# Kernel optimization log

Measured on AMD Instinct MI355X. Metric: run time of the kernel, lower is better.

Reference implementation:

```python
import jax, jax.numpy as jnp
import numpy as np

B, N, C = 2, 2048, 1024
H = 16
D = C // H  # head_dim = 64
SCALE = D ** -0.5


def setup_inputs() -> dict:
    key = jax.random.key(0)
    ks = jax.random.split(key, 9)
    s = C ** -0.5  # ~ torch Linear default init scale
    return {
        "x": jax.random.normal(ks[0], (B, N, C), dtype=jnp.float32),
        "Wq": jax.random.uniform(ks[1], (C, C), jnp.float32, -s, s),
        "bq": jax.random.uniform(ks[2], (C,), jnp.float32, -s, s),
        "Wk": jax.random.uniform(ks[3], (C, C), jnp.float32, -s, s),
        "bk": jax.random.uniform(ks[4], (C,), jnp.float32, -s, s),
        "Wv": jax.random.uniform(ks[5], (C, C), jnp.float32, -s, s),
        "bv": jax.random.uniform(ks[6], (C,), jnp.float32, -s, s),
        "Wo": jax.random.uniform(ks[7], (C, C), jnp.float32, -s, s),
        "bo": jax.random.uniform(ks[8], (C,), jnp.float32, -s, s),
    }


def reference(x, Wq, bq, Wk, bk, Wv, bv, Wo, bo):
    # Projections: [B,N,C] -> [B,H,N,D]
    def split_heads(t):
        return t.reshape(B, N, H, D).transpose(0, 2, 1, 3)

    q = split_heads(x @ Wq.T + bq)
    k = split_heads(x @ Wk.T + bk)
    v = split_heads(x @ Wv.T + bv)

    scores = jnp.einsum("bhnd,bhmd->bhnm", q, k) * SCALE  # [B,H,N,N]
    attn = jax.nn.softmax(scores, axis=-1)
    out = jnp.einsum("bhnm,bhmd->bhnd", attn, v)  # [B,H,N,D]
    out = out.transpose(0, 2, 1, 3).reshape(B, N, C)
    return out @ Wo.T + bo
```

## Files before the change

### kernel.cpp

```cpp
#include <hip/hip_runtime.h>
#include <stdint.h>


typedef _Float16 h8 __attribute__((ext_vector_type(8)));
typedef _Float16 h4 __attribute__((ext_vector_type(4)));
typedef float f4 __attribute__((ext_vector_type(4)));
typedef float f16f __attribute__((ext_vector_type(16)));
typedef uint32_t u32;
typedef u32 u32x4 __attribute__((ext_vector_type(4)));

#define AS1(p) ((const __attribute__((address_space(1))) void*)(p))
#define AS3(p) ((__attribute__((address_space(3))) void*)(p))

template <int ITERS>
__device__ __forceinline__ void stage128B(const _Float16* g, int ldk, _Float16* s, int tid) {
#pragma unroll
  for (int j = 0; j < ITERS; ++j) {
    int off = j * 4096 + tid * 16;
    int row = off >> 7;
    int ch = (off >> 4) & 7;
    int gch = ch ^ (row & 7);
    __builtin_amdgcn_global_load_lds(AS1(g + row * ldk + gch * 8), AS3(s + (off >> 1)), 16, 0, 0);
  }
}

__device__ __forceinline__ void stage_v(const _Float16* g, _Float16* s, int tid) {
#pragma unroll
  for (int j = 0; j < 2; ++j) {
    int off = j * 4096 + tid * 16;
    int row = off >> 7;
    int ch = (off >> 4) & 7;
    int gch = ch ^ (row & 7);
    __builtin_amdgcn_global_load_lds(AS1(g + row * 2048 + gch * 8), AS3(s + (off >> 1)), 16, 0, 0);
  }
}
__device__ __forceinline__ void stage_k(const _Float16* g, _Float16* s, int tid) {
#pragma unroll
  for (int j = 0; j < 2; ++j) {
    int off = j * 4096 + tid * 16;
    int row = off >> 7;
    int ch = (off >> 4) & 7;
    int gch = ch ^ ((row & 3) | ((row >> 1) & 4));
    __builtin_amdgcn_global_load_lds(AS1(g + row * 64 + gch * 8), AS3(s + (off >> 1)), 16, 0, 0);
  }
}

__device__ __forceinline__ h8 frag64(const _Float16* s, int row, int g) {
  return *(const h8*)(s + row * 64 + ((g ^ (row & 7)) << 3));
}

__global__ void cvt_all(const float* __restrict__ x, const float* __restrict__ Wq,
                        const float* __restrict__ Wk, const float* __restrict__ Wv,
                        const float* __restrict__ Wo, _Float16* __restrict__ xh,
                        _Float16* __restrict__ q, _Float16* __restrict__ k,
                        _Float16* __restrict__ v, _Float16* __restrict__ o) {
  int blk = blockIdx.x;
  const float* src; _Float16* dst; int off;
  if (blk < 4096)      { src = x;  dst = xh; off = blk; }
  else if (blk < 5120) { src = Wq; dst = q;  off = blk - 4096; }
  else if (blk < 6144) { src = Wk; dst = k;  off = blk - 5120; }
  else if (blk < 7168) { src = Wv; dst = v;  off = blk - 6144; }
  else                 { src = Wo; dst = o;  off = blk - 7168; }
  int i = off * 1024 + threadIdx.x * 4;
  f4 vv = *(const f4*)(src + i);
  h4 ov;
  ov[0] = (_Float16)vv[0]; ov[1] = (_Float16)vv[1]; ov[2] = (_Float16)vv[2]; ov[3] = (_Float16)vv[3];
  *(h4*)(dst + i) = ov;
}

__global__ __launch_bounds__(256, 3) void gemm_qkv(
    const _Float16* __restrict__ X,
    const _Float16* __restrict__ W0, const _Float16* __restrict__ W1, const _Float16* __restrict__ W2,
    const float* __restrict__ b0, const float* __restrict__ b1, const float* __restrict__ b2,
    _Float16* __restrict__ O0, _Float16* __restrict__ O1, _Float16* __restrict__ O2) {
  __shared__ _Float16 As[128 * 64];
  __shared__ _Float16 Bs[128 * 64];
  int z = blockIdx.z;
  const _Float16* W = (z == 0) ? W0 : (z == 1) ? W1 : W2;
  const float* bias = (z == 0) ? b0 : (z == 1) ? b1 : b2;

  int tid = threadIdx.x;
  int lane = tid & 63, wave = tid >> 6;
  int quad = lane >> 4, l15 = lane & 15;
  int wm = (wave >> 1) << 6, wn = (wave & 1) << 6;
  int m0 = blockIdx.y << 7, n0 = blockIdx.x << 7;

  f4 acc[4][4] = {};
  for (int k0 = 0; k0 < 1024; k0 += 64) {
    stage128B<4>(X + m0 * 1024 + k0, 1024, As, tid);
    stage128B<4>(W + n0 * 1024 + k0, 1024, Bs, tid);
    __syncthreads();
#pragma unroll
    for (int ks = 0; ks < 2; ++ks) {
      h8 af[4], bf[4];
#pragma unroll
      for (int i = 0; i < 4; ++i) af[i] = frag64(As, wm + i * 16 + l15, ks * 4 + quad);
#pragma unroll
      for (int i = 0; i < 4; ++i) bf[i] = frag64(Bs, wn + i * 16 + l15, ks * 4 + quad);
#pragma unroll
      for (int mi = 0; mi < 4; ++mi)
#pragma unroll
        for (int ni = 0; ni < 4; ++ni)
          acc[mi][ni] = __builtin_amdgcn_mfma_f32_16x16x32_f16(af[mi], bf[ni], acc[mi][ni], 0, 0, 0);
    }
    __syncthreads();
  }

  if (z == 2) {
#pragma unroll
    for (int mi = 0; mi < 4; ++mi) {
#pragma unroll
      for (int ni = 0; ni < 4; ++ni) {
        int o = n0 + wn + ni * 16 + l15;
        float bv = bias[o];
        int h = o >> 6, dd = o & 63;
        int m = m0 + wm + mi * 16 + quad * 4;
        int b = m >> 11, n = m & 2047;
        h4 v;
#pragma unroll
        for (int r = 0; r < 4; ++r) v[r] = (_Float16)(acc[mi][ni][r] + bv);
        *(h4*)(O2 + (((b * 16 + h) * 64 + dd) * 2048 + n)) = v;
      }
    }
  } else {
    float scale = (z == 0) ? 0.125f * 1.44269504089f : 1.0f;
    _Float16* Out = (z == 0) ? O0 : O1;
#pragma unroll
    for (int mi = 0; mi < 4; ++mi) {
#pragma unroll
      for (int ni = 0; ni < 4; ++ni) {
        int o = n0 + wn + ni * 16 + l15;
        float bv = bias[o];
        int h = o >> 6, d = o & 63;
#pragma unroll
        for (int r = 0; r < 4; ++r) {
          int m = m0 + wm + mi * 16 + quad * 4 + r;
          int b = m >> 11, n = m & 2047;
          float v = (acc[mi][ni][r] + bv) * scale;
          Out[(((b * 16 + h) * 2048 + n) << 6) + d] = (_Float16)v;
        }
      }
    }
  }
}

__global__ __launch_bounds__(256, 3) void gemm_out(
    const _Float16* __restrict__ A, const _Float16* __restrict__ W,
    const float* __restrict__ bias, float* __restrict__ Out) {
  __shared__ _Float16 As[128 * 64];
  __shared__ _Float16 Bs[64 * 64];
  int tid = threadIdx.x;
  int lane = tid & 63, wave = tid >> 6;
  int quad = lane >> 4, l15 = lane & 15;
  int wm = (wave >> 1) << 6, wn = (wave & 1) << 5;
  int m0 = blockIdx.y << 7, n0 = blockIdx.x << 6;

  f4 acc[4][2] = {};
  for (int k0 = 0; k0 < 1024; k0 += 64) {
    stage128B<4>(A + m0 * 1024 + k0, 1024, As, tid);
    stage128B<2>(W + n0 * 1024 + k0, 1024, Bs, tid);
    __syncthreads();
#pragma unroll
    for (int ks = 0; ks < 2; ++ks) {
      h8 af[4], bf[2];
#pragma unroll
      for (int i = 0; i < 4; ++i) af[i] = frag64(As, wm + i * 16 + l15, ks * 4 + quad);
#pragma unroll
      for (int i = 0; i < 2; ++i) bf[i] = frag64(Bs, wn + i * 16 + l15, ks * 4 + quad);
#pragma unroll
      for (int mi = 0; mi < 4; ++mi)
#pragma unroll
        for (int ni = 0; ni < 2; ++ni)
          acc[mi][ni] = __builtin_amdgcn_mfma_f32_16x16x32_f16(af[mi], bf[ni], acc[mi][ni], 0, 0, 0);
    }
    __syncthreads();
  }
#pragma unroll
  for (int mi = 0; mi < 4; ++mi) {
#pragma unroll
    for (int ni = 0; ni < 2; ++ni) {
      int o = n0 + wn + ni * 16 + l15;
      float bv = bias[o];
#pragma unroll
      for (int r = 0; r < 4; ++r) {
        int m = m0 + wm + mi * 16 + quad * 4 + r;
        Out[m * 1024 + o] = acc[mi][ni][r] + bv;
      }
    }
  }
}

__global__ __launch_bounds__(256, 2) void attn(
    const _Float16* __restrict__ Q, const _Float16* __restrict__ Kv,
    const _Float16* __restrict__ Vt, _Float16* __restrict__ AO) {
  __shared__ _Float16 smem[6 * 4096];
  _Float16* Ksb = smem;
  _Float16* Vsb = smem + 3 * 4096;

  int tid = threadIdx.x, lane = tid & 63, wave = tid >> 6;
  int h = lane >> 5, l31 = lane & 31;
  int p = wave & 1, qg = wave >> 1;

  int flat = blockIdx.y * 16 + blockIdx.x;
  int nid = (flat & 7) * 64 + (flat >> 3);
  int bh = nid >> 4, q0 = (nid & 15) << 7;

  const _Float16* Qb = Q + (bh * 2048 + q0 + qg * 64 + l31) * 64;
  h8 qf[2][4];
#pragma unroll
  for (int qs = 0; qs < 2; ++qs)
#pragma unroll
    for (int ks4 = 0; ks4 < 4; ++ks4)
      qf[qs][ks4] = *(const h8*)(Qb + qs * 32 * 64 + ks4 * 16 + h * 8);

  int krow = (l31 & 19) | ((l31 & 4) << 1) | ((l31 & 8) >> 1);
  int kbase = (p * 32 + krow) * 64;
  int kx = (krow & 3) | ((krow >> 1) & 4);
  int vx = l31 & 7;

  const _Float16* Kb = Kv + bh * 131072;
  const _Float16* Vb = Vt + bh * 131072;
  f16f oacc[2][2] = {};
  float lsum[2] = {0.f, 0.f};

  stage_k(Kb, Ksb, tid);
  stage_v(Vb, Vsb, tid);
  stage_k(Kb + 4096, Ksb + 4096, tid);
  stage_v(Vb + 64, Vsb + 4096, tid);

  int bp = 0;
  for (int ph = 0; ph < 32; ++ph) {
    if (ph < 31) {
      asm volatile("s_waitcnt vmcnt(4)\n\ts_barrier" ::: "memory");
    } else {
      asm volatile("s_waitcnt vmcnt(0)\n\ts_barrier" ::: "memory");
    }
    const _Float16* Kst = Ksb + bp * 4096;
    const _Float16* Vst = Vsb + bp * 4096;

    f16f sacc[2] = {};
#pragma unroll
    for (int ks4 = 0; ks4 < 4; ++ks4) {
      h8 kf = *(const h8*)(Kst + kbase + (((ks4 * 2 + h) ^ kx) << 3));
      sacc[0] = __builtin_amdgcn_mfma_f32_32x32x16_f16(kf, qf[0][ks4], sacc[0], 0, 0, 0);
      sacc[1] = __builtin_amdgcn_mfma_f32_32x32x16_f16(kf, qf[1][ks4], sacc[1], 0, 0, 0);
    }

    u32 pkw[2][8];
#pragma unroll
    for (int qs = 0; qs < 2; ++qs) {
#pragma unroll
      for (int i = 0; i < 8; ++i) {
        float pa = __builtin_amdgcn_exp2f(sacc[qs][2 * i]);
        float pb = __builtin_amdgcn_exp2f(sacc[qs][2 * i + 1]);
        lsum[qs] += pa + pb;
        pkw[qs][i] = __builtin_bit_cast(u32, __builtin_amdgcn_cvt_pkrtz(pa, pb));
      }
    }

#pragma unroll
    for (int s = 0; s < 2; ++s) {
      u32x4 pw0 = {pkw[0][4 * s], pkw[0][4 * s + 1], pkw[0][4 * s + 2], pkw[0][4 * s + 3]};
      u32x4 pw1 = {pkw[1][4 * s], pkw[1][4 * s + 1], pkw[1][4 * s + 2], pkw[1][4 * s + 3]};
      h8 pb0 = __builtin_bit_cast(h8, pw0);
      h8 pb1 = __builtin_bit_cast(h8, pw1);
      int ch = (((p << 2) | (s << 1) | h) ^ vx) << 3;
#pragma unroll
      for (int dt = 0; dt < 2; ++dt) {
        h8 vf = *(const h8*)(Vst + (dt * 32 + l31) * 64 + ch);
        oacc[0][dt] = __builtin_amdgcn_mfma_f32_32x32x16_f16(vf, pb0, oacc[0][dt], 0, 0, 0);
        oacc[1][dt] = __builtin_amdgcn_mfma_f32_32x32x16_f16(vf, pb1, oacc[1][dt], 0, 0, 0);
      }
    }

    if (ph < 30) {
      int sl = bp ? bp - 1 : 2;
      stage_k(Kb + (ph + 2) * 4096, Ksb + sl * 4096, tid);
      stage_v(Vb + (ph + 2) * 64, Vsb + sl * 4096, tid);
    }
    bp = (bp == 2) ? 0 : bp + 1;
  }

  __syncthreads();
  float* cb = (float*)smem;
  if (p) {
    float* w = cb + (qg * 64 + lane) * 66;
#pragma unroll
    for (int qs = 0; qs < 2; ++qs)
#pragma unroll
      for (int dt = 0; dt < 2; ++dt)
#pragma unroll
        for (int i = 0; i < 16; ++i) w[(qs * 2 + dt) * 16 + i] = oacc[qs][dt][i];
    w[64] = lsum[0];
    w[65] = lsum[1];
  }
  __syncthreads();
  if (!p) {
    const float* r = cb + (qg * 64 + lane) * 66;
#pragma unroll
    for (int qs = 0; qs < 2; ++qs)
#pragma unroll
      for (int dt = 0; dt < 2; ++dt)
#pragma unroll
        for (int i = 0; i < 16; ++i) oacc[qs][dt][i] += r[(qs * 2 + dt) * 16 + i];
    lsum[0] += r[64];
    lsum[1] += r[65];

    int b = bh >> 4, hh = bh & 15;
#pragma unroll
    for (int qs = 0; qs < 2; ++qs) {
      float l = lsum[qs] + __shfl_xor(lsum[qs], 32);
      float inv = 1.0f / l;
      int n = q0 + qg * 64 + qs * 32 + l31;
      _Float16* base = AO + (b * 2048 + n) * 1024 + hh * 64;
#pragma unroll
      for (int dt = 0; dt < 2; ++dt) {
#pragma unroll
        for (int b2 = 0; b2 < 4; ++b2) {
          h4 o;
#pragma unroll
          for (int a = 0; a < 4; ++a) o[a] = (_Float16)(oacc[qs][dt][b2 * 4 + a] * inv);
          *(h4*)(base + dt * 32 + b2 * 8 + h * 4) = o;
        }
      }
    }
  }
}

extern "C" void kernel_launch(void* const* d_in, const int* in_sizes, int n_in,
                              void* d_out, int out_size, void* d_ws, size_t ws_size,
                              hipStream_t stream) {
  const float* x = (const float*)d_in[0];
  const float* Wq = (const float*)d_in[1];
  const float* bq = (const float*)d_in[2];
  const float* Wk = (const float*)d_in[3];
  const float* bk = (const float*)d_in[4];
  const float* Wv = (const float*)d_in[5];
  const float* bv = (const float*)d_in[6];
  const float* Wo = (const float*)d_in[7];
  const float* bo = (const float*)d_in[8];
  float* out = (float*)d_out;

  char* w = (char*)d_ws;
  _Float16* xh  = (_Float16*)(w);
  _Float16* Wqh = (_Float16*)(w + (8u << 20));
  _Float16* Wkh = (_Float16*)(w + (10u << 20));
  _Float16* Wvh = (_Float16*)(w + (12u << 20));
  _Float16* Woh = (_Float16*)(w + (14u << 20));
  _Float16* Qh  = (_Float16*)(w + (16u << 20));
  _Float16* Kh  = (_Float16*)(w + (24u << 20));
  _Float16* Vth = (_Float16*)(w + (32u << 20));
  _Float16* AOh = xh;

  cvt_all<<<8192, 256, 0, stream>>>(x, Wq, Wk, Wv, Wo, xh, Wqh, Wkh, Wvh, Woh);
  gemm_qkv<<<dim3(8, 32, 3), 256, 0, stream>>>(xh, Wqh, Wkh, Wvh, bq, bk, bv, Qh, Kh, Vth);
  attn<<<dim3(16, 32), 256, 0, stream>>>(Qh, Kh, Vth, AOh);
  gemm_out<<<dim3(16, 32), 256, 0, stream>>>(AOh, Woh, bo, out);
}
```

Measured before the change: 182.7 us.

## Software-pipeline attention loop: overlap QK of next tile with softmax-PV of previous

Restructures the attention main loop to process two KV tiles per iteration with a 4-slot LDS ring. The QK MFMAs for one tile are interleaved with the exp/PV work of the prior tile, and s_setprio raises wave priority around MFMA bursts. The aim is to hide exp/VALU latency behind matrix work. In exchange it uses more LDS (32K halves instead of 24K), which may limit occupancy, and keeps more live score registers.

```diff
diff --git a/kernel.cpp b/kernel.cpp
--- a/kernel.cpp
+++ b/kernel.cpp
@@ -193,9 +193,9 @@
 __global__ __launch_bounds__(256, 2) void attn(
     const _Float16* __restrict__ Q, const _Float16* __restrict__ Kv,
     const _Float16* __restrict__ Vt, _Float16* __restrict__ AO) {
-  __shared__ _Float16 smem[6 * 4096];
+  __shared__ _Float16 smem[8 * 4096];
   _Float16* Ksb = smem;
-  _Float16* Vsb = smem + 3 * 4096;
+  _Float16* Vsb = smem + 4 * 4096;
 
   int tid = threadIdx.x, lane = tid & 63, wave = tid >> 6;
   int h = lane >> 5, l31 = lane & 31;
@@ -220,66 +220,85 @@
 
   const _Float16* Kb = Kv + bh * 131072;
   const _Float16* Vb = Vt + bh * 131072;
+
+  f16f zero = {};
   f16f oacc[2][2] = {};
-  float lsum[2] = {0.f, 0.f};
+  float lsum0 = 0.f, lsum1 = 0.f;
+
+  auto SMPV = [&](const f16f& sa, const f16f& sb, const _Float16* Vst) {
+    u32 pkw0[8], pkw1[8];
+#pragma unroll
+    for (int i = 0; i < 8; ++i) {
+      float pa = __builtin_amdgcn_exp2f(sa[2 * i]);
+      float pb = __builtin_amdgcn_exp2f(sa[2 * i + 1]);
+      lsum0 += pa + pb;
+      pkw0[i] = __builtin_bit_cast(u32, __builtin_amdgcn_cvt_pkrtz(pa, pb));
+      float pc = __builtin_amdgcn_exp2f(sb[2 * i]);
+      float pd = __builtin_amdgcn_exp2f(sb[2 * i + 1]);
+      lsum1 += pc + pd;
+      pkw1[i] = __builtin_bit_cast(u32, __builtin_amdgcn_cvt_pkrtz(pc, pd));
+    }
+#pragma unroll
+    for (int s = 0; s < 2; ++s) {
+      u32x4 pw0 = {pkw0[4 * s], pkw0[4 * s + 1], pkw0[4 * s + 2], pkw0[4 * s + 3]};
+      u32x4 pw1 = {pkw1[4 * s], pkw1[4 * s + 1], pkw1[4 * s + 2], pkw1[4 * s + 3]};
+      h8 pb0 = __builtin_bit_cast(h8, pw0);
+      h8 pb1 = __builtin_bit_cast(h8, pw1);
+      int ch = (((p << 2) | (s << 1) | h) ^ vx) << 3;
+      __builtin_amdgcn_s_setprio(1);
+#pragma unroll
+      for (int dt = 0; dt < 2; ++dt) {
+        h8 vf = *(const h8*)(Vst + (dt * 32 + l31) * 64 + ch);
+        oacc[0][dt] = __builtin_amdgcn_mfma_f32_32x32x16_f16(vf, pb0, oacc[0][dt], 0, 0, 0);
+        oacc[1][dt] = __builtin_amdgcn_mfma_f32_32x32x16_f16(vf, pb1, oacc[1][dt], 0, 0, 0);
+      }
+      __builtin_amdgcn_s_setprio(0);
+    }
+  };
+
+  auto QK = [&](const _Float16* Kst, f16f& s0, f16f& s1) {
+    s0 = zero; s1 = zero;
+    __builtin_amdgcn_s_setprio(1);
+#pragma unroll
+    for (int ks4 = 0; ks4 < 4; ++ks4) {
+      h8 kf = *(const h8*)(Kst + kbase + (((ks4 * 2 + h) ^ kx) << 3));
+      s0 = __builtin_amdgcn_mfma_f32_32x32x16_f16(kf, qf[0][ks4], s0, 0, 0, 0);
+      s1 = __builtin_amdgcn_mfma_f32_32x32x16_f16(kf, qf[1][ks4], s1, 0, 0, 0);
+    }
+    __builtin_amdgcn_s_setprio(0);
+  };
 
   stage_k(Kb, Ksb, tid);
   stage_v(Vb, Vsb, tid);
   stage_k(Kb + 4096, Ksb + 4096, tid);
   stage_v(Vb + 64, Vsb + 4096, tid);
 
-  int bp = 0;
-  for (int ph = 0; ph < 32; ++ph) {
-    if (ph < 31) {
+  f16f sA0 = zero, sA1 = zero, sB0 = zero, sB1 = zero;
+
+  for (int it = 0; it < 16; ++it) {
+    int base = (it & 1) << 1;
+    int ob = base ^ 2;
+    int ph0 = it << 1;
+
+    asm volatile("s_waitcnt vmcnt(4)\n\ts_barrier" ::: "memory");
+    if (it < 15) {
+      stage_k(Kb + (ph0 + 2) * 4096, Ksb + ob * 4096, tid);
+      stage_v(Vb + (ph0 + 2) * 64, Vsb + ob * 4096, tid);
+    }
+    QK(Ksb + base * 4096, sA0, sA1);
+    if (it > 0) SMPV(sB0, sB1, Vsb + (ob | 1) * 4096);
+
+    if (it < 15) {
       asm volatile("s_waitcnt vmcnt(4)\n\ts_barrier" ::: "memory");
+      stage_k(Kb + (ph0 + 3) * 4096, Ksb + (ob | 1) * 4096, tid);
+      stage_v(Vb + (ph0 + 3) * 64, Vsb + (ob | 1) * 4096, tid);
     } else {
       asm volatile("s_waitcnt vmcnt(0)\n\ts_barrier" ::: "memory");
     }
-    const _Float16* Kst = Ksb + bp * 4096;
-    const _Float16* Vst = Vsb + bp * 4096;
-
-    f16f sacc[2] = {};
-#pragma unroll
-    for (int ks4 = 0; ks4 < 4; ++ks4) {
-      h8 kf = *(const h8*)(Kst + kbase + (((ks4 * 2 + h) ^ kx) << 3));
-      sacc[0] = __builtin_amdgcn_mfma_f32_32x32x16_f16(kf, qf[0][ks4], sacc[0], 0, 0, 0);
-      sacc[1] = __builtin_amdgcn_mfma_f32_32x32x16_f16(kf, qf[1][ks4], sacc[1], 0, 0, 0);
-    }
-
-    u32 pkw[2][8];
-#pragma unroll
-    for (int qs = 0; qs < 2; ++qs) {
-#pragma unroll
-      for (int i = 0; i < 8; ++i) {
-        float pa = __builtin_amdgcn_exp2f(sacc[qs][2 * i]);
-        float pb = __builtin_amdgcn_exp2f(sacc[qs][2 * i + 1]);
-        lsum[qs] += pa + pb;
-        pkw[qs][i] = __builtin_bit_cast(u32, __builtin_amdgcn_cvt_pkrtz(pa, pb));
-      }
-    }
-
-#pragma unroll
-    for (int s = 0; s < 2; ++s) {
-      u32x4 pw0 = {pkw[0][4 * s], pkw[0][4 * s + 1], pkw[0][4 * s + 2], pkw[0][4 * s + 3]};
-      u32x4 pw1 = {pkw[1][4 * s], pkw[1][4 * s + 1], pkw[1][4 * s + 2], pkw[1][4 * s + 3]};
-      h8 pb0 = __builtin_bit_cast(h8, pw0);
-      h8 pb1 = __builtin_bit_cast(h8, pw1);
-      int ch = (((p << 2) | (s << 1) | h) ^ vx) << 3;
-#pragma unroll
-      for (int dt = 0; dt < 2; ++dt) {
-        h8 vf = *(const h8*)(Vst + (dt * 32 + l31) * 64 + ch);
-        oacc[0][dt] = __builtin_amdgcn_mfma_f32_32x32x16_f16(vf, pb0, oacc[0][dt], 0, 0, 0);
-        oacc[1][dt] = __builtin_amdgcn_mfma_f32_32x32x16_f16(vf, pb1, oacc[1][dt], 0, 0, 0);
-      }
-    }
-
-    if (ph < 30) {
-      int sl = bp ? bp - 1 : 2;
-      stage_k(Kb + (ph + 2) * 4096, Ksb + sl * 4096, tid);
-      stage_v(Vb + (ph + 2) * 64, Vsb + sl * 4096, tid);
-    }
-    bp = (bp == 2) ? 0 : bp + 1;
-  }
+    QK(Ksb + (base | 1) * 4096, sB0, sB1);
+    SMPV(sA0, sA1, Vsb + base * 4096);
+  }
+  SMPV(sB0, sB1, Vsb + 3 * 4096);
 
   __syncthreads();
   float* cb = (float*)smem;
@@ -291,8 +310,8 @@
       for (int dt = 0; dt < 2; ++dt)
 #pragma unroll
         for (int i = 0; i < 16; ++i) w[(qs * 2 + dt) * 16 + i] = oacc[qs][dt][i];
-    w[64] = lsum[0];
-    w[65] = lsum[1];
+    w[64] = lsum0;
+    w[65] = lsum1;
   }
   __syncthreads();
   if (!p) {
@@ -303,16 +322,17 @@
       for (int dt = 0; dt < 2; ++dt)
 #pragma unroll
         for (int i = 0; i < 16; ++i) oacc[qs][dt][i] += r[(qs * 2 + dt) * 16 + i];
-    lsum[0] += r[64];
-    lsum[1] += r[65];
+    lsum0 += r[64];
+    lsum1 += r[65];
 
     int b = bh >> 4, hh = bh & 15;
 #pragma unroll
     for (int qs = 0; qs < 2; ++qs) {
-      float l = lsum[qs] + __shfl_xor(lsum[qs], 32);
+      float ls = qs ? lsum1 : lsum0;
+      float l = ls + __shfl_xor(ls, 32);
       float inv = 1.0f / l;
       int n = q0 + qg * 64 + qs * 32 + l31;
-      _Float16* base = AO + (b * 2048 + n) * 1024 + hh * 64;
+      _Float16* base_ = AO + (b * 2048 + n) * 1024 + hh * 64;
 #pragma unroll
       for (int dt = 0; dt < 2; ++dt) {
 #pragma unroll
@@ -320,7 +340,7 @@
           h4 o;
 #pragma unroll
           for (int a = 0; a < 4; ++a) o[a] = (_Float16)(oacc[qs][dt][b2 * 4 + a] * inv);
-          *(h4*)(base + dt * 32 + b2 * 8 + h * 4) = o;
+          *(h4*)(base_ + dt * 32 + b2 * 8 + h * 4) = o;
         }
       }
     }
```

New measurement: 173.6 us. 1.05x faster.

## Double-buffer LDS tiles in QKV and output projection GEMMs

Applied to the files above, without the earlier changes.

Both projection GEMMs now keep two LDS buffers. They prefetch the next K-tile via global_load_lds while computing on the current one, with a single barrier per iteration instead of two. This is meant to hide global-load latency behind MFMA work. It doubles LDS use, and gemm_qkv's launch bound drops to 2 blocks per CU, which may reduce occupancy.

```diff
diff --git a/kernel.cpp b/kernel.cpp
--- a/kernel.cpp
+++ b/kernel.cpp
@@ -68,13 +68,13 @@
   *(h4*)(dst + i) = ov;
 }
 
-__global__ __launch_bounds__(256, 3) void gemm_qkv(
+__global__ __launch_bounds__(256, 2) void gemm_qkv(
     const _Float16* __restrict__ X,
     const _Float16* __restrict__ W0, const _Float16* __restrict__ W1, const _Float16* __restrict__ W2,
     const float* __restrict__ b0, const float* __restrict__ b1, const float* __restrict__ b2,
     _Float16* __restrict__ O0, _Float16* __restrict__ O1, _Float16* __restrict__ O2) {
-  __shared__ _Float16 As[128 * 64];
-  __shared__ _Float16 Bs[128 * 64];
+  __shared__ _Float16 As[2][128 * 64];
+  __shared__ _Float16 Bs[2][128 * 64];
   int z = blockIdx.z;
   const _Float16* W = (z == 0) ? W0 : (z == 1) ? W1 : W2;
   const float* bias = (z == 0) ? b0 : (z == 1) ? b1 : b2;
@@ -85,25 +85,31 @@
   int wm = (wave >> 1) << 6, wn = (wave & 1) << 6;
   int m0 = blockIdx.y << 7, n0 = blockIdx.x << 7;
 
+  stage128B<4>(X + m0 * 1024, 1024, As[0], tid);
+  stage128B<4>(W + n0 * 1024, 1024, Bs[0], tid);
+
   f4 acc[4][4] = {};
-  for (int k0 = 0; k0 < 1024; k0 += 64) {
-    stage128B<4>(X + m0 * 1024 + k0, 1024, As, tid);
-    stage128B<4>(W + n0 * 1024 + k0, 1024, Bs, tid);
+  for (int k = 0; k < 16; ++k) {
     __syncthreads();
+    if (k < 15) {
+      stage128B<4>(X + m0 * 1024 + (k + 1) * 64, 1024, As[(k + 1) & 1], tid);
+      stage128B<4>(W + n0 * 1024 + (k + 1) * 64, 1024, Bs[(k + 1) & 1], tid);
+    }
+    const _Float16* Asl = As[k & 1];
+    const _Float16* Bsl = Bs[k & 1];
 #pragma unroll
     for (int ks = 0; ks < 2; ++ks) {
       h8 af[4], bf[4];
 #pragma unroll
-      for (int i = 0; i < 4; ++i) af[i] = frag64(As, wm + i * 16 + l15, ks * 4 + quad);
-#pragma unroll
-      for (int i = 0; i < 4; ++i) bf[i] = frag64(Bs, wn + i * 16 + l15, ks * 4 + quad);
+      for (int i = 0; i < 4; ++i) af[i] = frag64(Asl, wm + i * 16 + l15, ks * 4 + quad);
+#pragma unroll
+      for (int i = 0; i < 4; ++i) bf[i] = frag64(Bsl, wn + i * 16 + l15, ks * 4 + quad);
 #pragma unroll
       for (int mi = 0; mi < 4; ++mi)
 #pragma unroll
         for (int ni = 0; ni < 4; ++ni)
           acc[mi][ni] = __builtin_amdgcn_mfma_f32_16x16x32_f16(af[mi], bf[ni], acc[mi][ni], 0, 0, 0);
     }
-    __syncthreads();
   }
 
   if (z == 2) {
@@ -147,33 +153,39 @@
 __global__ __launch_bounds__(256, 3) void gemm_out(
     const _Float16* __restrict__ A, const _Float16* __restrict__ W,
     const float* __restrict__ bias, float* __restrict__ Out) {
-  __shared__ _Float16 As[128 * 64];
-  __shared__ _Float16 Bs[64 * 64];
+  __shared__ _Float16 As[2][128 * 64];
+  __shared__ _Float16 Bs[2][64 * 64];
   int tid = threadIdx.x;
   int lane = tid & 63, wave = tid >> 6;
   int quad = lane >> 4, l15 = lane & 15;
   int wm = (wave >> 1) << 6, wn = (wave & 1) << 5;
   int m0 = blockIdx.y << 7, n0 = blockIdx.x << 6;
 
+  stage128B<4>(A + m0 * 1024, 1024, As[0], tid);
+  stage128B<2>(W + n0 * 1024, 1024, Bs[0], tid);
+
   f4 acc[4][2] = {};
-  for (int k0 = 0; k0 < 1024; k0 += 64) {
-    stage128B<4>(A + m0 * 1024 + k0, 1024, As, tid);
-    stage128B<2>(W + n0 * 1024 + k0, 1024, Bs, tid);
+  for (int k = 0; k < 16; ++k) {
     __syncthreads();
+    if (k < 15) {
+      stage128B<4>(A + m0 * 1024 + (k + 1) * 64, 1024, As[(k + 1) & 1], tid);
+      stage128B<2>(W + n0 * 1024 + (k + 1) * 64, 1024, Bs[(k + 1) & 1], tid);
+    }
+    const _Float16* Asl = As[k & 1];
+    const _Float16* Bsl = Bs[k & 1];
 #pragma unroll
     for (int ks = 0; ks < 2; ++ks) {
       h8 af[4], bf[2];
 #pragma unroll
-      for (int i = 0; i < 4; ++i) af[i] = frag64(As, wm + i * 16 + l15, ks * 4 + quad);
-#pragma unroll
-      for (int i = 0; i < 2; ++i) bf[i] = frag64(Bs, wn + i * 16 + l15, ks * 4 + quad);
+      for (int i = 0; i < 4; ++i) af[i] = frag64(Asl, wm + i * 16 + l15, ks * 4 + quad);
+#pragma unroll
+      for (int i = 0; i < 2; ++i) bf[i] = frag64(Bsl, wn + i * 16 + l15, ks * 4 + quad);
 #pragma unroll
       for (int mi = 0; mi < 4; ++mi)
 #pragma unroll
         for (int ni = 0; ni < 2; ++ni)
           acc[mi][ni] = __builtin_amdgcn_mfma_f32_16x16x32_f16(af[mi], bf[ni], acc[mi][ni], 0, 0, 0);
     }
-    __syncthreads();
   }
 #pragma unroll
   for (int mi = 0; mi < 4; ++mi) {
```

Result: slower. 205.5 us (+12.5%).
